# Performance work log

Hardware: AMD Instinct MI355X
Metric: run time of the kernel (lower is better)

## Reference

```python
import jax, jax.numpy as jnp
import numpy as np

D_MODEL = 1024
N_HEADS = 16
D_K = D_MODEL // N_HEADS
SEQ = 4096
BATCH = 1
THETA = 10000.0


def setup_inputs() -> dict:
    key = jax.random.key(0)
    ks = jax.random.split(key, 5)
    scale = 0.02
    x = jax.random.normal(ks[0], (BATCH, SEQ, D_MODEL), dtype=jnp.float32)
    token_positions = jnp.broadcast_to(jnp.arange(SEQ, dtype=jnp.int64 if jax.config.jax_enable_x64 else jnp.int32)[None, :], (BATCH, SEQ))
    Wq = jax.random.normal(ks[1], (D_MODEL, D_MODEL), dtype=jnp.float32) * scale
    Wk = jax.random.normal(ks[2], (D_MODEL, D_MODEL), dtype=jnp.float32) * scale
    Wv = jax.random.normal(ks[3], (D_MODEL, D_MODEL), dtype=jnp.float32) * scale
    Wo = jax.random.normal(ks[4], (D_MODEL, D_MODEL), dtype=jnp.float32) * scale
    return {"x": x, "token_positions": token_positions, "Wq": Wq, "Wk": Wk, "Wv": Wv, "Wo": Wo}


def _apply_rope(t, token_positions, theta=THETA):
    # t: (b, h, s, d_k); token_positions: (b, s)
    d_k = t.shape[-1]
    inv_freq = theta ** (-jnp.arange(0, d_k, 2, dtype=jnp.float32) / d_k)  # (d_k/2,)
    ang = token_positions.astype(jnp.float32)[:, :, None] * inv_freq  # (b, s, d_k/2)
    cos = jnp.cos(ang)[:, None, :, :]  # (b, 1, s, d_k/2)
    sin = jnp.sin(ang)[:, None, :, :]
    te, to = t[..., 0::2], t[..., 1::2]
    re = te * cos - to * sin
    ro = te * sin + to * cos
    # interleave back: (..., d_k/2, 2) -> (..., d_k)
    return jnp.stack([re, ro], axis=-1).reshape(t.shape)


def reference(x, token_positions, Wq, Wk, Wv, Wo):
    b, s, d_model = x.shape
    h, d_k = N_HEADS, D_K
    q = (x @ Wq.T).reshape(b, s, h, d_k).transpose(0, 2, 1, 3)  # (b,h,s,d_k)
    k = (x @ Wk.T).reshape(b, s, h, d_k).transpose(0, 2, 1, 3)
    v = (x @ Wv.T).reshape(b, s, h, d_k).transpose(0, 2, 1, 3)
    q = _apply_rope(q, token_positions)
    k = _apply_rope(k, token_positions)
    scores = jnp.einsum('bhqd,bhkd->bhqk', q, k) / jnp.sqrt(jnp.float32(d_k))
    causal = jnp.tril(jnp.ones((s, s), dtype=bool))[None, None]
    scores = jnp.where(causal, scores, jnp.float32(-1e9))
    attn = jax.nn.softmax(scores, axis=-1)
    out = jnp.einsum('bhqk,bhkd->bhqd', attn, v)  # (b,h,s,d_k)
    out = out.transpose(0, 2, 1, 3).reshape(b, s, d_model)
    return out @ Wo.T
```

## Files before the change

### kernel.cpp

```cpp
#include <hip/hip_runtime.h>
#include <hip/hip_bf16.h>
#include <math.h>


#define SEQ 4096
#define DM  1024
#define NH  16
#define DK  64

typedef __attribute__((ext_vector_type(8))) short short8;
typedef __attribute__((ext_vector_type(4))) float floatx4;
typedef __attribute__((ext_vector_type(16))) float floatx16;
typedef __attribute__((ext_vector_type(4))) short short4v;

static __device__ __forceinline__ short f2bf(float f) {
    __hip_bfloat16 h = __float2bfloat16(f);
    return __builtin_bit_cast(short, h);
}

static __device__ __forceinline__ float fast_exp2(float x) {
#if __has_builtin(__builtin_amdgcn_exp2f)
    return __builtin_amdgcn_exp2f(x);
#else
    return exp2f(x);
#endif
}

static __device__ __forceinline__ short8 load8_f32_as_bf16(const float* p) {
    float4 a = *reinterpret_cast<const float4*>(p);
    float4 b = *reinterpret_cast<const float4*>(p + 4);
    short8 s;
    s[0] = f2bf(a.x); s[1] = f2bf(a.y); s[2] = f2bf(a.z); s[3] = f2bf(a.w);
    s[4] = f2bf(b.x); s[5] = f2bf(b.y); s[6] = f2bf(b.z); s[7] = f2bf(b.w);
    return s;
}

static __device__ __forceinline__ void gl2lds16(const __hip_bfloat16* g, short* l) {
    __builtin_amdgcn_global_load_lds(
        (const __attribute__((address_space(1))) unsigned int*)g,
        (__attribute__((address_space(3))) unsigned int*)l, 16, 0, 0);
}

static __device__ __forceinline__ int read_pos(const int* tp32, int s) {
    return (tp32[1] == 1) ? tp32[s] : tp32[2 * s];
}

__global__ __launch_bounds__(256) void prep_kernel(
    const float* __restrict__ x,  const float* __restrict__ Wq,
    const float* __restrict__ Wk, const float* __restrict__ Wv,
    const int* __restrict__ tp,
    __hip_bfloat16* __restrict__ xb,  __hip_bfloat16* __restrict__ Wqb,
    __hip_bfloat16* __restrict__ Wkb, __hip_bfloat16* __restrict__ Wvb,
    float2* __restrict__ tab)
{
    int b = blockIdx.x;
    if (b < 3584) {
        const float* src; __hip_bfloat16* dst; int off;
        if (b < 2048)      { src = x;  dst = xb;  off = b; }
        else if (b < 2560) { src = Wq; dst = Wqb; off = b - 2048; }
        else if (b < 3072) { src = Wk; dst = Wkb; off = b - 2560; }
        else               { src = Wv; dst = Wvb; off = b - 3072; }
        size_t i = (size_t)off * 256 + threadIdx.x;
        short8 v = load8_f32_as_bf16(src + i * 8);
        *reinterpret_cast<short8*>((short*)dst + i * 8) = v;
    } else {
        int idx = (b - 3584) * 256 + threadIdx.x;
        if (idx < SEQ * 32) {
            int s = idx >> 5, pair = idx & 31;
            float inv_freq = exp2f(-(float)(2 * pair) * (13.287712379549449f / 64.f));
            float sn, cs;
            sincosf((float)read_pos(tp, s) * inv_freq, &sn, &cs);
            tab[idx] = make_float2(cs, sn);
        }
    }
}

__global__ __launch_bounds__(256) void qkv_rope_kernel(
    const __hip_bfloat16* __restrict__ xb,
    const float2* __restrict__ tab,
    const __hip_bfloat16* __restrict__ Wqb,
    const __hip_bfloat16* __restrict__ Wkb,
    const __hip_bfloat16* __restrict__ Wvb,
    __hip_bfloat16* __restrict__ q_ws,
    __hip_bfloat16* __restrict__ k_ws,
    __hip_bfloat16* __restrict__ vt_ws)
{
    __shared__ __align__(16) short pool[17408];
    short* As = pool;
    short* Bs = pool + 8192;

    const int by = blockIdx.y;
    const int wsel = by >> 3;
    const __hip_bfloat16* W = (wsel == 0) ? Wqb : (wsel == 1 ? Wkb : Wvb);
    const int nloc0 = (by & 7) * 128;
    const int m0 = blockIdx.x * 128;

    const int t = threadIdx.x;
    const int lane = t & 63;
    const int w = t >> 6;
    const int quad = lane >> 4;
    const int ln = lane & 15;
    const int wm = (w >> 1) * 64;
    const int wn = (w & 1) * 64;

    floatx4 acc[4][4];
    #pragma unroll
    for (int i = 0; i < 4; i++)
        #pragma unroll
        for (int j = 0; j < 4; j++) acc[i][j] = (floatx4){0.f, 0.f, 0.f, 0.f};

    for (int k0 = 0; k0 < DM; k0 += 64) {
        #pragma unroll
        for (int it = 0; it < 4; it++) {
            int row = w * 32 + it * 8 + (lane >> 3);
            int sg = (lane & 7) ^ (row & 7);
            gl2lds16(&xb[(size_t)(m0 + row) * DM + k0 + sg * 8], &As[(w * 32 + it * 8) * 64]);
            gl2lds16(&W[(size_t)(nloc0 + row) * DM + k0 + sg * 8], &Bs[(w * 32 + it * 8) * 64]);
        }
        __syncthreads();

        short8 af[4][2], bfr[4][2];
        #pragma unroll
        for (int i = 0; i < 4; i++)
            #pragma unroll
            for (int kc = 0; kc < 2; kc++)
                af[i][kc] = *reinterpret_cast<const short8*>(
                    &As[(wm + i * 16 + ln) * 64 + (((kc * 4 + quad) ^ (ln & 7)) << 3)]);
        #pragma unroll
        for (int j = 0; j < 4; j++)
            #pragma unroll
            for (int kc = 0; kc < 2; kc++)
                bfr[j][kc] = *reinterpret_cast<const short8*>(
                    &Bs[(wn + j * 16 + ln) * 64 + (((kc * 4 + quad) ^ (ln & 7)) << 3)]);

        #pragma unroll
        for (int kc = 0; kc < 2; kc++)
            #pragma unroll
            for (int i = 0; i < 4; i++)
                #pragma unroll
                for (int j = 0; j < 4; j++)
                    acc[i][j] = __builtin_amdgcn_mfma_f32_16x16x32_bf16(
                        af[i][kc], bfr[j][kc], acc[i][j], 0, 0, 0);
        __syncthreads();
    }

    if (wsel < 2) {
        __hip_bfloat16* dst = (wsel == 0) ? q_ws : k_ws;
        const float qscale = (wsel == 0) ? 0.18033688011112042f : 1.0f;
        #pragma unroll
        for (int j = 0; j < 4; j++) {
            int cnl = wn + j * 16 + ln;
            int pair = ((nloc0 + cnl) & 63) >> 1;
            #pragma unroll
            for (int i = 0; i < 4; i++) {
                int rowl = wm + i * 16 + quad * 4;
                #pragma unroll
                for (int r = 0; r < 4; r++) {
                    float2 t2 = tab[(size_t)(m0 + rowl + r) * 32 + pair];
                    float val = acc[i][j][r];
                    float partner = __shfl_xor(val, 1, 64);
                    float res = val * t2.x + (((lane & 1) ? partner : -partner) * t2.y);
                    pool[(rowl + r) * 136 + cnl] = f2bf(res * qscale);
                }
            }
        }
        __syncthreads();
        int row = t >> 1, half = t & 1;
        size_t gbase = (size_t)(m0 + row) * DM + nloc0 + half * 64;
        #pragma unroll
        for (int c = 0; c < 8; c++)
            *reinterpret_cast<short8*>(&dst[gbase + c * 8]) =
                *reinterpret_cast<const short8*>(&pool[row * 136 + half * 64 + c * 8]);
    } else {
        #pragma unroll
        for (int j = 0; j < 4; j++) {
            int cnl = wn + j * 16 + ln;
            #pragma unroll
            for (int i = 0; i < 4; i++) {
                int s0 = wm + i * 16 + quad * 4;
                #pragma unroll
                for (int r = 0; r < 4; r++)
                    pool[cnl * 136 + s0 + r] = f2bf(acc[i][j][r]);
            }
        }
        __syncthreads();
        int cnl = t >> 1, sh = t & 1;
        size_t base = (size_t)(nloc0 + cnl) * SEQ + m0 + sh * 64;
        #pragma unroll
        for (int c = 0; c < 8; c++)
            *reinterpret_cast<short8*>(&vt_ws[base + c * 8]) =
                *reinterpret_cast<const short8*>(&pool[cnl * 136 + sh * 64 + c * 8]);
    }
}

__global__ __launch_bounds__(512, 1) void attn_kernel(
    const __hip_bfloat16* __restrict__ q_ws,
    const __hip_bfloat16* __restrict__ k_ws,
    const __hip_bfloat16* __restrict__ vt_ws,
    __hip_bfloat16* __restrict__ o_ws)
{
    __shared__ __align__(16) short Kt[2][128 * 64];
    __shared__ __align__(16) short Vt[2][64 * 128];

    const int bid = (int)blockIdx.x;
    const int head = bid & 15;
    const int jp = bid >> 4;

    const int t = threadIdx.x;
    const int lane = t & 63;
    const int w = t >> 6;
    const int ww = w & 3;
    const int kh = w >> 2;
    const int hi = lane >> 5;
    const int l31 = lane & 31;

    auto stage = [&](int b, int kb) {
        #pragma unroll
        for (int i = 0; i < 2; i++) {
            int r = w * 16 + i * 8 + (lane >> 3);
            int keyloc = (r & ~12) | ((r & 4) << 1) | ((r & 8) >> 1);
            int g = (lane & 7) ^ (r & 7);
            gl2lds16(&k_ws[(size_t)(kb + keyloc) * DM + head * 64 + g * 8],
                     &Kt[b][(w * 16 + i * 8) * 64]);
        }
        #pragma unroll
        for (int i = 0; i < 2; i++) {
            int d = w * 8 + i * 4 + (lane >> 4);
            int g = (lane & 15) ^ (d & 7);
            gl2lds16(&vt_ws[(size_t)(head * 64 + d) * SEQ + kb + g * 8],
                     &Vt[b][(w * 8 + i * 4) * 128]);
        }
    };

    #pragma unroll 1
    for (int pass = 0; pass < 2; pass++) {
        const int tile = pass ? jp : (31 - jp);
        const int nstep = tile + 1;
        const int q0 = tile * 128 + ww * 32;

        short8 qf[4];
        #pragma unroll
        for (int c = 0; c < 4; c++)
            qf[c] = *reinterpret_cast<const short8*>(
                &q_ws[(size_t)(q0 + l31) * DM + head * 64 + c * 16 + hi * 8]);

        floatx16 accO[2];
        #pragma unroll
        for (int db = 0; db < 2; db++)
            #pragma unroll
            for (int i = 0; i < 16; i++) accO[db][i] = 0.f;
        float l = 0.f;

        __syncthreads();
        stage(0, 0);
        int buf = 0;
        for (int st = 0; st < nstep; st++) {
            __syncthreads();
            if (st + 1 < nstep) stage(buf ^ 1, (st + 1) * 128);
            const bool last = (st == nstep - 1);

            #pragma unroll
            for (int kk = 0; kk < 2; kk++) {
                const int kb32 = kh * 2 + kk;
                if (!(last && kb32 > ww)) {
                    const int krow = kb32 * 32 + l31;
                    short8 kfr[4];
                    #pragma unroll
                    for (int kc = 0; kc < 4; kc++) {
                        int g = (kc * 2 + hi) ^ (krow & 7);
                        kfr[kc] = *reinterpret_cast<const short8*>(&Kt[buf][krow * 64 + g * 8]);
                    }
                    floatx16 s;
                    #pragma unroll
                    for (int i = 0; i < 16; i++) s[i] = 0.f;
                    __builtin_amdgcn_s_setprio(1);
                    #pragma unroll
                    for (int kc = 0; kc < 4; kc++)
                        s = __builtin_amdgcn_mfma_f32_32x32x16_bf16(kfr[kc], qf[kc], s, 0, 0, 0);
                    __builtin_amdgcn_s_setprio(0);

                    if (last) {
                        #pragma unroll
                        for (int r = 0; r < 16; r++) {
                            int key_l = kb32 * 32 + (r & 7) + 2 * (r & 8) + 8 * hi;
                            if (key_l > ww * 32 + l31) s[r] = -1e9f;
                        }
                    }
                    float p[16];
                    #pragma unroll
                    for (int r = 0; r < 16; r++) { p[r] = fast_exp2(s[r]); l += p[r]; }

                    union { short8 v; short e[8]; } pb[2];
                    #pragma unroll
                    for (int c = 0; c < 2; c++)
                        #pragma unroll
                        for (int e8 = 0; e8 < 8; e8++)
                            pb[c].e[e8] = f2bf(p[c * 8 + e8]);

                    #pragma unroll
                    for (int db = 0; db < 2; db++) {
                        const int vrow = db * 32 + l31;
                        short8 vfr[2];
                        #pragma unroll
                        for (int c = 0; c < 2; c++) {
                            int g = (kb32 * 4 + c * 2 + hi) ^ (vrow & 7);
                            vfr[c] = *reinterpret_cast<const short8*>(&Vt[buf][vrow * 128 + g * 8]);
                        }
                        __builtin_amdgcn_s_setprio(1);
                        accO[db] = __builtin_amdgcn_mfma_f32_32x32x16_bf16(vfr[0], pb[0].v, accO[db], 0, 0, 0);
                        accO[db] = __builtin_amdgcn_mfma_f32_32x32x16_bf16(vfr[1], pb[1].v, accO[db], 0, 0, 0);
                        __builtin_amdgcn_s_setprio(0);
                    }
                }
            }
            buf ^= 1;
        }

        float* xf = (float*)Vt;
        const int xbase = (ww * 64 + lane) * 19;
        __syncthreads();
        if (kh == 1) {
            #pragma unroll
            for (int i = 0; i < 16; i++) xf[xbase + i] = accO[0][i];
            xf[xbase + 16] = l;
        }
        __syncthreads();
        if (kh == 0) {
            #pragma unroll
            for (int i = 0; i < 16; i++) accO[0][i] += xf[xbase + i];
            l += xf[xbase + 16];
        }
        __syncthreads();
        if (kh == 1) {
            #pragma unroll
            for (int i = 0; i < 16; i++) xf[xbase + i] = accO[1][i];
        }
        __syncthreads();
        if (kh == 0) {
            #pragma unroll
            for (int i = 0; i < 16; i++) accO[1][i] += xf[xbase + i];
        }

        float lf = l + __shfl_xor(l, 32, 64);
        float rl = 1.f / lf;

        short* pool = (short*)Kt;
        if (kh == 0) {
            const int qrow = ww * 32 + l31;
            #pragma unroll
            for (int db = 0; db < 2; db++)
                #pragma unroll
                for (int j = 0; j < 4; j++) {
                    union { short4v v; short e[4]; } g;
                    #pragma unroll
                    for (int m = 0; m < 4; m++)
                        g.e[m] = f2bf(accO[db][j * 4 + m] * rl);
                    int dcol = db * 32 + j * 8 + 4 * hi;
                    *reinterpret_cast<short4v*>(&pool[qrow * 68 + dcol]) = g.v;
                }
        }
        __syncthreads();

        {
            int r = t >> 2, q4 = t & 3;
            size_t gb = (size_t)(tile * 128 + r) * DM + head * 64 + q4 * 16;
            union { short8 v8; short4v h[2]; } u;
            u.h[0] = *reinterpret_cast<const short4v*>(&pool[r * 68 + q4 * 16]);
            u.h[1] = *reinterpret_cast<const short4v*>(&pool[r * 68 + q4 * 16 + 4]);
            *reinterpret_cast<short8*>(&o_ws[gb]) = u.v8;
            union { short8 v8; short4v h[2]; } u2;
            u2.h[0] = *reinterpret_cast<const short4v*>(&pool[r * 68 + q4 * 16 + 8]);
            u2.h[1] = *reinterpret_cast<const short4v*>(&pool[r * 68 + q4 * 16 + 12]);
            *reinterpret_cast<short8*>(&o_ws[gb + 8]) = u2.v8;
        }
    }
}

__global__ __launch_bounds__(256) void oproj_kernel(
    const __hip_bfloat16* __restrict__ o_in,
    const float* __restrict__ Wo,
    float* __restrict__ out)
{
    __shared__ __align__(16) char smem[24576];
    short* As = (short*)smem;
    short* Bs = As + 8192;
    float* fpool = (float*)smem;

    const int m0 = blockIdx.x * 128;
    const int n0 = blockIdx.y * 64;

    const int t = threadIdx.x;
    const int lane = t & 63;
    const int w = t >> 6;
    const int quad = lane >> 4;
    const int ln = lane & 15;
    const int wm = (w >> 1) * 64;
    const int wn = (w & 1) * 32;

    floatx4 acc[4][2];
    #pragma unroll
    for (int i = 0; i < 4; i++)
        #pragma unroll
        for (int j = 0; j < 2; j++) acc[i][j] = (floatx4){0.f, 0.f, 0.f, 0.f};

    for (int k0 = 0; k0 < DM; k0 += 64) {
        #pragma unroll
        for (int it = 0; it < 4; it++) {
            int row = w * 32 + it * 8 + (lane >> 3);
            int sg = (lane & 7) ^ (row & 7);
            gl2lds16(&o_in[(size_t)(m0 + row) * DM + k0 + sg * 8], &As[(w * 32 + it * 8) * 64]);
        }
        #pragma unroll
        for (int p = 0; p < 2; p++) {
            int r = (t >> 3) + p * 32;
            int sg2 = t & 7;
            *reinterpret_cast<short8*>(&Bs[r * 64 + ((sg2 ^ (r & 7)) << 3)]) =
                load8_f32_as_bf16(&Wo[(size_t)(n0 + r) * DM + k0 + sg2 * 8]);
        }
        __syncthreads();

        short8 af[4][2], bfr[2][2];
        #pragma unroll
        for (int i = 0; i < 4; i++)
            #pragma unroll
            for (int kc = 0; kc < 2; kc++)
                af[i][kc] = *reinterpret_cast<const short8*>(
                    &As[(wm + i * 16 + ln) * 64 + (((kc * 4 + quad) ^ (ln & 7)) << 3)]);
        #pragma unroll
        for (int j = 0; j < 2; j++)
            #pragma unroll
            for (int kc = 0; kc < 2; kc++)
                bfr[j][kc] = *reinterpret_cast<const short8*>(
                    &Bs[(wn + j * 16 + ln) * 64 + (((kc * 4 + quad) ^ (ln & 7)) << 3)]);

        #pragma unroll
        for (int kc = 0; kc < 2; kc++)
            #pragma unroll
            for (int i = 0; i < 4; i++)
                #pragma unroll
                for (int j = 0; j < 2; j++)
                    acc[i][j] = __builtin_amdgcn_mfma_f32_16x16x32_bf16(
                        af[i][kc], bfr[j][kc], acc[i][j], 0, 0, 0);
        __syncthreads();
    }

    #pragma unroll
    for (int ph = 0; ph < 2; ph++) {
        if ((w >> 1) == ph) {
            #pragma unroll
            for (int j = 0; j < 2; j++)
                #pragma unroll
                for (int i = 0; i < 4; i++) {
                    int rl = i * 16 + quad * 4;
                    #pragma unroll
                    for (int r = 0; r < 4; r++)
                        fpool[(rl + r) * 68 + wn + j * 16 + ln] = acc[i][j][r];
                }
        }
        __syncthreads();
        int row = t >> 2;
        int c0 = (t & 3) * 16;
        size_t gbase = (size_t)(m0 + ph * 64 + row) * DM + n0 + c0;
        #pragma unroll
        for (int c = 0; c < 4; c++)
            *reinterpret_cast<float4*>(&out[gbase + c * 4]) =
                *reinterpret_cast<const float4*>(&fpool[row * 68 + c0 + c * 4]);
        __syncthreads();
    }
}

extern "C" void kernel_launch(void* const* d_in, const int* in_sizes, int n_in,
                              void* d_out, int out_size, void* d_ws, size_t ws_size,
                              hipStream_t stream) {
    const float* x  = (const float*)d_in[0];
    const int* tp   = (const int*)d_in[1];
    const float* Wq = (const float*)d_in[2];
    const float* Wk = (const float*)d_in[3];
    const float* Wv = (const float*)d_in[4];
    const float* Wo = (const float*)d_in[5];
    float* out = (float*)d_out;

    char* ws = (char*)d_ws;
    const size_t MB = 1024 * 1024;
    __hip_bfloat16* xb    = (__hip_bfloat16*)(ws);
    __hip_bfloat16* q_ws  = (__hip_bfloat16*)(ws + 8  * MB);
    __hip_bfloat16* k_ws  = (__hip_bfloat16*)(ws + 16 * MB);
    __hip_bfloat16* vt_ws = (__hip_bfloat16*)(ws + 24 * MB);
    __hip_bfloat16* o_ws  = xb;
    __hip_bfloat16* Wqb = (__hip_bfloat16*)d_out;
    __hip_bfloat16* Wkb = Wqb + (size_t)DM * DM;
    __hip_bfloat16* Wvb = Wkb + (size_t)DM * DM;
    float2* tab = (float2*)((char*)d_out + 6 * MB);

    prep_kernel<<<4096, 256, 0, stream>>>(x, Wq, Wk, Wv, tp, xb, Wqb, Wkb, Wvb, tab);
    qkv_rope_kernel<<<dim3(32, 24), 256, 0, stream>>>(xb, tab, Wqb, Wkb, Wvb, q_ws, k_ws, vt_ws);
    attn_kernel<<<256, 512, 0, stream>>>(q_ws, k_ws, vt_ws, o_ws);
    oproj_kernel<<<dim3(32, 16), 256, 0, stream>>>(o_ws, Wo, out);
}
```

Baseline: 210.4 us.

## Split attention key tile across four wave groups with 1024-thread blocks

The attention block grows from 512 to 1024 threads. Each 128-key tile is now split four ways across wave groups (one 32-key chunk per wave) instead of two ways, so each wave does half the per-step work. A two-level LDS reduction of the partial O accumulators and row sums replaces the single-step combine, and the staging and output store are redistributed over the larger thread count. This aims to add latency hiding and MFMA parallelism per CU. In exchange it adds more barriers and reduction traffic, and more waves sit idle on the causal last step.

```diff
diff --git a/kernel.cpp b/kernel.cpp
--- a/kernel.cpp
+++ b/kernel.cpp
@@ -193,7 +193,7 @@
     }
 }
 
-__global__ __launch_bounds__(512, 1) void attn_kernel(
+__global__ __launch_bounds__(1024, 1) void attn_kernel(
     const __hip_bfloat16* __restrict__ q_ws,
     const __hip_bfloat16* __restrict__ k_ws,
     const __hip_bfloat16* __restrict__ vt_ws,
@@ -210,25 +210,23 @@
     const int lane = t & 63;
     const int w = t >> 6;
     const int ww = w & 3;
-    const int kh = w >> 2;
+    const int kq = w >> 2;
     const int hi = lane >> 5;
     const int l31 = lane & 31;
 
     auto stage = [&](int b, int kb) {
-        #pragma unroll
-        for (int i = 0; i < 2; i++) {
-            int r = w * 16 + i * 8 + (lane >> 3);
+        {
+            int r = w * 8 + (lane >> 3);
             int keyloc = (r & ~12) | ((r & 4) << 1) | ((r & 8) >> 1);
             int g = (lane & 7) ^ (r & 7);
             gl2lds16(&k_ws[(size_t)(kb + keyloc) * DM + head * 64 + g * 8],
-                     &Kt[b][(w * 16 + i * 8) * 64]);
-        }
-        #pragma unroll
-        for (int i = 0; i < 2; i++) {
-            int d = w * 8 + i * 4 + (lane >> 4);
+                     &Kt[b][(w * 8) * 64]);
+        }
+        {
+            int d = w * 4 + (lane >> 4);
             int g = (lane & 15) ^ (d & 7);
             gl2lds16(&vt_ws[(size_t)(head * 64 + d) * SEQ + kb + g * 8],
-                     &Vt[b][(w * 8 + i * 4) * 128]);
+                     &Vt[b][(w * 4) * 128]);
         }
     };
 
@@ -259,93 +257,111 @@
             if (st + 1 < nstep) stage(buf ^ 1, (st + 1) * 128);
             const bool last = (st == nstep - 1);
 
-            #pragma unroll
-            for (int kk = 0; kk < 2; kk++) {
-                const int kb32 = kh * 2 + kk;
-                if (!(last && kb32 > ww)) {
-                    const int krow = kb32 * 32 + l31;
-                    short8 kfr[4];
+            if (!(last && kq > ww)) {
+                const int kb32 = kq;
+                const int krow = kb32 * 32 + l31;
+                short8 kfr[4];
+                #pragma unroll
+                for (int kc = 0; kc < 4; kc++) {
+                    int g = (kc * 2 + hi) ^ (krow & 7);
+                    kfr[kc] = *reinterpret_cast<const short8*>(&Kt[buf][krow * 64 + g * 8]);
+                }
+                floatx16 s;
+                #pragma unroll
+                for (int i = 0; i < 16; i++) s[i] = 0.f;
+                __builtin_amdgcn_s_setprio(1);
+                #pragma unroll
+                for (int kc = 0; kc < 4; kc++)
+                    s = __builtin_amdgcn_mfma_f32_32x32x16_bf16(kfr[kc], qf[kc], s, 0, 0, 0);
+                __builtin_amdgcn_s_setprio(0);
+
+                if (last) {
                     #pragma unroll
-                    for (int kc = 0; kc < 4; kc++) {
-                        int g = (kc * 2 + hi) ^ (krow & 7);
-                        kfr[kc] = *reinterpret_cast<const short8*>(&Kt[buf][krow * 64 + g * 8]);
-                    }
-                    floatx16 s;
-                    #pragma unroll
-                    for (int i = 0; i < 16; i++) s[i] = 0.f;
-                    __builtin_amdgcn_s_setprio(1);
-                    #pragma unroll
-                    for (int kc = 0; kc < 4; kc++)
-                        s = __builtin_amdgcn_mfma_f32_32x32x16_bf16(kfr[kc], qf[kc], s, 0, 0, 0);
-                    __builtin_amdgcn_s_setprio(0);
-
-                    if (last) {
-                        #pragma unroll
-                        for (int r = 0; r < 16; r++) {
-                            int key_l = kb32 * 32 + (r & 7) + 2 * (r & 8) + 8 * hi;
-                            if (key_l > ww * 32 + l31) s[r] = -1e9f;
-                        }
-                    }
-                    float p[16];
-                    #pragma unroll
-                    for (int r = 0; r < 16; r++) { p[r] = fast_exp2(s[r]); l += p[r]; }
-
-                    union { short8 v; short e[8]; } pb[2];
-                    #pragma unroll
-                    for (int c = 0; c < 2; c++)
-                        #pragma unroll
-                        for (int e8 = 0; e8 < 8; e8++)
-                            pb[c].e[e8] = f2bf(p[c * 8 + e8]);
-
-                    #pragma unroll
-                    for (int db = 0; db < 2; db++) {
-                        const int vrow = db * 32 + l31;
-                        short8 vfr[2];
-                        #pragma unroll
-                        for (int c = 0; c < 2; c++) {
-                            int g = (kb32 * 4 + c * 2 + hi) ^ (vrow & 7);
-                            vfr[c] = *reinterpret_cast<const short8*>(&Vt[buf][vrow * 128 + g * 8]);
-                        }
-                        __builtin_amdgcn_s_setprio(1);
-                        accO[db] = __builtin_amdgcn_mfma_f32_32x32x16_bf16(vfr[0], pb[0].v, accO[db], 0, 0, 0);
-                        accO[db] = __builtin_amdgcn_mfma_f32_32x32x16_bf16(vfr[1], pb[1].v, accO[db], 0, 0, 0);
-                        __builtin_amdgcn_s_setprio(0);
+                    for (int r = 0; r < 16; r++) {
+                        int key_l = kb32 * 32 + (r & 7) + 2 * (r & 8) + 8 * hi;
+                        if (key_l > ww * 32 + l31) s[r] = -1e9f;
                     }
                 }
+                float p[16];
+                #pragma unroll
+                for (int r = 0; r < 16; r++) { p[r] = fast_exp2(s[r]); l += p[r]; }
+
+                union { short8 v; short e[8]; } pb[2];
+                #pragma unroll
+                for (int c = 0; c < 2; c++)
+                    #pragma unroll
+                    for (int e8 = 0; e8 < 8; e8++)
+                        pb[c].e[e8] = f2bf(p[c * 8 + e8]);
+
+                #pragma unroll
+                for (int db = 0; db < 2; db++) {
+                    const int vrow = db * 32 + l31;
+                    short8 vfr[2];
+                    #pragma unroll
+                    for (int c = 0; c < 2; c++) {
+                        int g = (kb32 * 4 + c * 2 + hi) ^ (vrow & 7);
+                        vfr[c] = *reinterpret_cast<const short8*>(&Vt[buf][vrow * 128 + g * 8]);
+                    }
+                    __builtin_amdgcn_s_setprio(1);
+                    accO[db] = __builtin_amdgcn_mfma_f32_32x32x16_bf16(vfr[0], pb[0].v, accO[db], 0, 0, 0);
+                    accO[db] = __builtin_amdgcn_mfma_f32_32x32x16_bf16(vfr[1], pb[1].v, accO[db], 0, 0, 0);
+                    __builtin_amdgcn_s_setprio(0);
+                }
             }
             buf ^= 1;
         }
 
-        float* xf = (float*)Vt;
-        const int xbase = (ww * 64 + lane) * 19;
-        __syncthreads();
-        if (kh == 1) {
-            #pragma unroll
-            for (int i = 0; i < 16; i++) xf[xbase + i] = accO[0][i];
-            xf[xbase + 16] = l;
-        }
-        __syncthreads();
-        if (kh == 0) {
-            #pragma unroll
-            for (int i = 0; i < 16; i++) accO[0][i] += xf[xbase + i];
-            l += xf[xbase + 16];
-        }
-        __syncthreads();
-        if (kh == 1) {
-            #pragma unroll
-            for (int i = 0; i < 16; i++) xf[xbase + i] = accO[1][i];
-        }
-        __syncthreads();
-        if (kh == 0) {
-            #pragma unroll
-            for (int i = 0; i < 16; i++) accO[1][i] += xf[xbase + i];
+        float* scrK = (float*)Kt;
+        float* scrV = (float*)Vt;
+        __syncthreads();
+        {
+            const int slot = (ww * 2 + (kq & 1)) * 64 + lane;
+            if (kq >= 2) {
+                #pragma unroll
+                for (int i = 0; i < 16; i++) scrK[i * 512 + slot] = accO[0][i];
+                scrV[slot] = l;
+            }
+            __syncthreads();
+            if (kq < 2) {
+                #pragma unroll
+                for (int i = 0; i < 16; i++) accO[0][i] += scrK[i * 512 + slot];
+                l += scrV[slot];
+            }
+            __syncthreads();
+            if (kq >= 2) {
+                #pragma unroll
+                for (int i = 0; i < 16; i++) scrK[i * 512 + slot] = accO[1][i];
+            }
+            __syncthreads();
+            if (kq < 2) {
+                #pragma unroll
+                for (int i = 0; i < 16; i++) accO[1][i] += scrK[i * 512 + slot];
+            }
+            __syncthreads();
+            const int slot2 = ww * 64 + lane;
+            if (kq == 1) {
+                #pragma unroll
+                for (int i = 0; i < 16; i++) scrK[i * 256 + slot2] = accO[0][i];
+                #pragma unroll
+                for (int i = 0; i < 16; i++) scrK[(16 + i) * 256 + slot2] = accO[1][i];
+                scrV[slot2] = l;
+            }
+            __syncthreads();
+            if (kq == 0) {
+                #pragma unroll
+                for (int i = 0; i < 16; i++) accO[0][i] += scrK[i * 256 + slot2];
+                #pragma unroll
+                for (int i = 0; i < 16; i++) accO[1][i] += scrK[(16 + i) * 256 + slot2];
+                l += scrV[slot2];
+            }
         }
 
         float lf = l + __shfl_xor(l, 32, 64);
         float rl = 1.f / lf;
 
+        __syncthreads();
         short* pool = (short*)Kt;
-        if (kh == 0) {
+        if (kq == 0) {
             const int qrow = ww * 32 + l31;
             #pragma unroll
             for (int db = 0; db < 2; db++)
@@ -362,16 +378,12 @@
         __syncthreads();
 
         {
-            int r = t >> 2, q4 = t & 3;
-            size_t gb = (size_t)(tile * 128 + r) * DM + head * 64 + q4 * 16;
+            int r = t >> 3, c8 = t & 7;
+            size_t gb = (size_t)(tile * 128 + r) * DM + head * 64 + c8 * 8;
             union { short8 v8; short4v h[2]; } u;
-            u.h[0] = *reinterpret_cast<const short4v*>(&pool[r * 68 + q4 * 16]);
-            u.h[1] = *reinterpret_cast<const short4v*>(&pool[r * 68 + q4 * 16 + 4]);
+            u.h[0] = *reinterpret_cast<const short4v*>(&pool[r * 68 + c8 * 8]);
+            u.h[1] = *reinterpret_cast<const short4v*>(&pool[r * 68 + c8 * 8 + 4]);
             *reinterpret_cast<short8*>(&o_ws[gb]) = u.v8;
-            union { short8 v8; short4v h[2]; } u2;
-            u2.h[0] = *reinterpret_cast<const short4v*>(&pool[r * 68 + q4 * 16 + 8]);
-            u2.h[1] = *reinterpret_cast<const short4v*>(&pool[r * 68 + q4 * 16 + 12]);
-            *reinterpret_cast<short8*>(&o_ws[gb + 8]) = u2.v8;
         }
     }
 }
@@ -494,6 +506,6 @@
 
     prep_kernel<<<4096, 256, 0, stream>>>(x, Wq, Wk, Wv, tp, xb, Wqb, Wkb, Wvb, tab);
     qkv_rope_kernel<<<dim3(32, 24), 256, 0, stream>>>(xb, tab, Wqb, Wkb, Wvb, q_ws, k_ws, vt_ws);
-    attn_kernel<<<256, 512, 0, stream>>>(q_ws, k_ws, vt_ws, o_ws);
+    attn_kernel<<<256, 1024, 0, stream>>>(q_ws, k_ws, vt_ws, o_ws);
     oproj_kernel<<<dim3(32, 16), 256, 0, stream>>>(o_ws, Wo, out);
 }
```

Result: faster. 205.0 us (-2.6%).
